# Performance work log

Measured on AMD Instinct MI355X. Metric: run time of the kernel, lower is better.

Reference implementation:

```python
import jax, jax.numpy as jnp
import numpy as np

H = 128
EPS = 1e-5

def _layernorm(x, g, b):
    mu = jnp.mean(x, axis=-1, keepdims=True)
    var = jnp.mean(jnp.square(x - mu), axis=-1, keepdims=True)
    return (x - mu) * jax.lax.rsqrt(var + EPS) * g + b

def _block(x, W, b, g, be):
    # Linear -> LayerNorm -> ReLU (dropout is identity at eval)
    return jax.nn.relu(_layernorm(x @ W + b, g, be))

def setup_inputs() -> dict:
    key = jax.random.key(0)
    ks = jax.random.split(key, 12)
    B, N, C = 32, 4096, 512
    s1 = 1.0 / np.sqrt(H)
    s2 = 1.0 / np.sqrt(2 * H)
    return {
        "fine_features": jax.random.normal(ks[0], (B, N, H), jnp.float32),
        "coarse_features": jax.random.normal(ks[1], (B, C, H), jnp.float32),
        "global_features": jax.random.normal(ks[2], (B, N, H), jnp.float32),
        "atom_to_coarse": jax.random.randint(ks[3], (B, N), 0, 600),  # some >= C (invalid)
        "W_pool": jax.random.uniform(ks[4], (H, H), jnp.float32, -s1, s1),
        "b_pool": jnp.zeros((H,), jnp.float32),
        "g_pool": jnp.ones((H,), jnp.float32),
        "be_pool": jnp.zeros((H,), jnp.float32),
        "W_unpool": jax.random.uniform(ks[5], (H, H), jnp.float32, -s1, s1),
        "b_unpool": jnp.zeros((H,), jnp.float32),
        "g_unpool": jnp.ones((H,), jnp.float32),
        "be_unpool": jnp.zeros((H,), jnp.float32),
        "W_gate": jax.random.uniform(ks[6], (2 * H, H), jnp.float32, -s2, s2),
        "b_gate": jnp.zeros((H,), jnp.float32),
        "W_glob": jax.random.uniform(ks[7], (2 * H, H), jnp.float32, -s2, s2),
        "b_glob": jnp.zeros((H,), jnp.float32),
        "g_glob": jnp.ones((H,), jnp.float32),
        "be_glob": jnp.zeros((H,), jnp.float32),
    }

def reference(fine_features, coarse_features, global_features, atom_to_coarse,
              W_pool, b_pool, g_pool, be_pool,
              W_unpool, b_unpool, g_unpool, be_unpool,
              W_gate, b_gate, W_glob, b_glob, g_glob, be_glob):
    B, N, Hd = fine_features.shape
    C = coarse_features.shape[1]
    idx = atom_to_coarse
    valid = (idx >= 0) & (idx < C)                      # [B,N]

    # ---- batched scatter-add pooling via flat segment_sum ----
    # invalid atoms routed to extra bucket C per batch element
    seg = jnp.where(valid, idx, C) + jnp.arange(B, dtype=idx.dtype)[:, None] * (C + 1)
    pooled = jax.ops.segment_sum(fine_features.reshape(B * N, Hd),
                                 seg.reshape(-1), num_segments=B * (C + 1))
    pooled = pooled.reshape(B, C + 1, Hd)[:, :C]        # [B,C,H]
    counts = jax.ops.segment_sum(valid.reshape(-1).astype(jnp.float32),
                                 seg.reshape(-1), num_segments=B * (C + 1))
    counts = counts.reshape(B, C + 1)[:, :C]
    coarse_from_fine = pooled / jnp.maximum(counts, 1.0)[..., None]
    coarse_from_fine = _block(coarse_from_fine, W_pool, b_pool, g_pool, be_pool)

    # ---- gather unpooling ----
    safe = jnp.where(valid, idx, 0)
    gathered = jnp.take_along_axis(coarse_features, safe[:, :, None], axis=1)  # [B,N,H]
    fine_from_coarse = jnp.where(valid[..., None], gathered, 0.0)
    fine_from_coarse = _block(fine_from_coarse, W_unpool, b_unpool, g_unpool, be_unpool)

    # ---- gated fusion ----
    fine_gate = jax.nn.sigmoid(jnp.concatenate([fine_features, fine_from_coarse], -1) @ W_gate + b_gate)
    fine_updated = fine_gate * fine_features + (1.0 - fine_gate) * fine_from_coarse
    coarse_gate = jax.nn.sigmoid(jnp.concatenate([coarse_features, coarse_from_fine], -1) @ W_gate + b_gate)
    coarse_updated = coarse_gate * coarse_features + (1.0 - coarse_gate) * coarse_from_fine

    # ---- global injection ----
    fine_wg = _block(jnp.concatenate([fine_updated, global_features], -1), W_glob, b_glob, g_glob, be_glob)
    fine_updated = fine_updated + 0.1 * fine_wg
    glob_c = jnp.broadcast_to(jnp.mean(global_features, axis=1, keepdims=True), (B, C, Hd))
    coarse_wg = _block(jnp.concatenate([coarse_updated, glob_c], -1), W_glob, b_glob, g_glob, be_glob)
    coarse_updated = coarse_updated + 0.1 * coarse_wg
    return (fine_updated, coarse_updated)
```

## Files before the change

kernel.cpp:

```cpp
#include <hip/hip_runtime.h>

typedef __bf16 bf16;
typedef bf16 bf16x8 __attribute__((ext_vector_type(8)));
typedef float f32x4 __attribute__((ext_vector_type(4)));

#define TPP 512
#define TPM 256
#define UPAD 136

#define NPOOL 1024
#define NGM   512
#define NPREP 64
#define NM1   256
#define NM0   2048

__device__ inline unsigned short f2bf(float f){
  union{ bf16 h; unsigned short u; } v; v.h = (bf16)f; return v.u;
}
__device__ inline float bf2f(unsigned short u){
  union{ unsigned short u; bf16 h; } v; v.u = u; return (float)v.h;
}
__device__ inline unsigned int pk2(float a, float b){
  return (unsigned int)f2bf(a) | ((unsigned int)f2bf(b) << 16);
}
union BF8 { bf16x8 v; unsigned int u[4]; };
__device__ inline bf16x8 pack8(float4 a, float4 b){
  BF8 r; r.u[0] = pk2(a.x, a.y); r.u[1] = pk2(a.z, a.w);
  r.u[2] = pk2(b.x, b.y); r.u[3] = pk2(b.z, b.w); return r.v;
}

__device__ inline void gll16(const unsigned short* g, unsigned short* l){
  __builtin_amdgcn_global_load_lds(
      (const __attribute__((address_space(1))) unsigned int*)g,
      (__attribute__((address_space(3))) unsigned int*)l, 16, 0, 0);
}
__device__ inline void stage_win(const unsigned short* __restrict__ src,
                                 unsigned short* half, int tid){
#pragma unroll
  for (int i = 0; i < 4; ++i){
    int p = (tid + i*TPM)*8;
    gll16(src + p, half + p);
  }
}

__device__ inline void gemm_win(const bf16x8 a[2], const unsigned short* half,
                                f32x4 acc[8], int lane){
#pragma unroll
  for (int kk = 0; kk < 2; ++kk){
    bf16x8 av = a[kk];
#pragma unroll
    for (int n = 0; n < 8; ++n){
      bf16x8 bv = *(const bf16x8*)(half + (size_t)((n*2 + kk)*512) + lane*8);
      acc[n] = __builtin_amdgcn_mfma_f32_16x16x32_bf16(av, bv, acc[n], 0, 0, 0);
    }
  }
}

__device__ inline void rowstats(const f32x4 acc[8], const float bia[8],
                                float mean[4], float rstd[4]){
#pragma unroll
  for (int ri = 0; ri < 4; ++ri){
    float s = 0.f, q = 0.f;
#pragma unroll
    for (int n = 0; n < 8; ++n){
      float z = acc[n][ri] + bia[n];
      s += z; q += z*z;
    }
#pragma unroll
    for (int m = 1; m < 16; m <<= 1){ s += __shfl_xor(s, m); q += __shfl_xor(q, m); }
    mean[ri] = s * (1.f/128.f);
    float var = q * (1.f/128.f) - mean[ri]*mean[ri];
    rstd[ri] = rsqrtf(var + 1e-5f);
  }
}

struct PoolSh {
  int sidx[4096];
  int rows[4096];
  int cnt[16], off[17], woff[16];
};
struct GmeanSh { float4 part4[16][32]; };
union PreSh { PoolSh p; GmeanSh g; };

__device__ void pool_body(PoolSh& sh, int pid,
                          const float* __restrict__ fine,
                          const int* __restrict__ idx,
                          unsigned short* __restrict__ pooled){
  int b = pid >> 5, g = pid & 31;
  int c0 = g * 16;
  int tid = threadIdx.x;
  const int* idx_b = idx + b*4096;
#pragma unroll
  for (int i = 0; i < 2; ++i)
    ((int4*)sh.sidx)[tid + i*TPP] = ((const int4*)idx_b)[tid + i*TPP];
  if (tid < 16) sh.cnt[tid] = 0;
  __syncthreads();
  for (int i = tid; i < 4096; i += TPP){
    unsigned d = (unsigned)(sh.sidx[i] - c0);
    if (d < 16u) atomicAdd(&sh.cnt[d], 1);
  }
  __syncthreads();
  if (tid == 0){
    int s = 0;
#pragma unroll
    for (int j = 0; j < 16; ++j){ sh.off[j] = s; s += sh.cnt[j]; }
    sh.off[16] = s;
  }
  __syncthreads();
  if (tid < 16) sh.woff[tid] = sh.off[tid];
  __syncthreads();
  for (int i = tid; i < 4096; i += TPP){
    unsigned d = (unsigned)(sh.sidx[i] - c0);
    if (d < 16u){ int p = atomicAdd(&sh.woff[d], 1); sh.rows[p] = i; }
  }
  __syncthreads();
  int hw = tid >> 5, l32 = tid & 31;
  const float* fb = fine + (size_t)b*4096*128;
  int o0 = sh.off[hw], o1 = sh.off[hw+1];
  float4 s = {0.f, 0.f, 0.f, 0.f};
  int m = o0;
  for (; m + 3 < o1; m += 4){
    float4 v0 = *((const float4*)(fb + (size_t)sh.rows[m+0]*128) + l32);
    float4 v1 = *((const float4*)(fb + (size_t)sh.rows[m+1]*128) + l32);
    float4 v2 = *((const float4*)(fb + (size_t)sh.rows[m+2]*128) + l32);
    float4 v3 = *((const float4*)(fb + (size_t)sh.rows[m+3]*128) + l32);
    s.x += (v0.x + v1.x) + (v2.x + v3.x);
    s.y += (v0.y + v1.y) + (v2.y + v3.y);
    s.z += (v0.z + v1.z) + (v2.z + v3.z);
    s.w += (v0.w + v1.w) + (v2.w + v3.w);
  }
  for (; m < o1; ++m){
    float4 v = *((const float4*)(fb + (size_t)sh.rows[m]*128) + l32);
    s.x += v.x; s.y += v.y; s.z += v.z; s.w += v.w;
  }
  float inv = 1.f / fmaxf((float)(o1 - o0), 1.f);
  unsigned short* po = pooled + ((size_t)(b*512 + c0 + hw))*128 + l32*4;
  uint2 w2; w2.x = pk2(s.x*inv, s.y*inv); w2.y = pk2(s.z*inv, s.w*inv);
  *(uint2*)po = w2;
}

__device__ void gmean_body(GmeanSh& sh, int gid,
                           const float* __restrict__ glob,
                           float* __restrict__ gmean){
  int b = gid >> 4, ch = gid & 15;
  int tid = threadIdx.x;
  int c4 = tid & 31, rg = tid >> 5;
  const float* gb = glob + ((size_t)b*4096 + ch*256)*128;
  float4 a = {0.f, 0.f, 0.f, 0.f};
#pragma unroll
  for (int i = 0; i < 16; ++i){
    int r = rg + i*16;
    float4 v = *(const float4*)(gb + (size_t)r*128 + c4*4);
    a.x += v.x; a.y += v.y; a.z += v.z; a.w += v.w;
  }
  sh.part4[rg][c4] = a;
  __syncthreads();
  if (tid < 32){
    float4 s = sh.part4[0][tid];
#pragma unroll
    for (int g = 1; g < 16; ++g){
      float4 v = sh.part4[g][tid];
      s.x += v.x; s.y += v.y; s.z += v.z; s.w += v.w;
    }
    float* gm = gmean + b*128 + tid*4;
    atomicAdd(&gm[0], s.x); atomicAdd(&gm[1], s.y);
    atomicAdd(&gm[2], s.z); atomicAdd(&gm[3], s.w);
  }
}

__device__ void prep_body(int e,
                          const float* __restrict__ Wp, const float* __restrict__ Wu,
                          const float* __restrict__ Wg, const float* __restrict__ Wgl,
                          unsigned short* __restrict__ WfP, unsigned short* __restrict__ WfU,
                          unsigned short* __restrict__ WfG, unsigned short* __restrict__ WfGl){
  int j = e & 7, lane = (e >> 3) & 63, frag = e >> 9;
  int kk = frag & 1, nblk = (frag >> 1) & 7, c = frag >> 4;
  int il = lane & 15, lg = lane >> 4;
  int col = nblk*16 + il;
  int k = c*64 + kk*32 + lg*8 + j;
  if (e < 16384){
    WfP[e] = f2bf(Wp[k*128 + col]);
    WfU[e] = f2bf(Wu[k*128 + col]);
  }
  WfG[e]  = f2bf(Wg[k*128 + col]);
  WfGl[e] = f2bf(Wgl[k*128 + col]);
}

__global__ __launch_bounds__(TPP) void k_pre(
    const float* __restrict__ fine, const int* __restrict__ idx,
    const float* __restrict__ glob,
    const float* __restrict__ Wp, const float* __restrict__ Wu,
    const float* __restrict__ Wg, const float* __restrict__ Wgl,
    unsigned short* __restrict__ pooled, float* __restrict__ gmean,
    unsigned short* __restrict__ WfP, unsigned short* __restrict__ WfU,
    unsigned short* __restrict__ WfG, unsigned short* __restrict__ WfGl){
  __shared__ __align__(16) PreSh sh;
  int bid = blockIdx.x;
  if (bid < NPOOL)             pool_body(sh.p, bid, fine, idx, pooled);
  else if (bid < NPOOL + NGM)  gmean_body(sh.g, bid - NPOOL, glob, gmean);
  else                         prep_body((bid - NPOOL - NGM)*TPP + threadIdx.x,
                                         Wp, Wu, Wg, Wgl, WfP, WfU, WfG, WfGl);
}

struct MegaSh {
  unsigned short wb[2][8192];
  unsigned short ubuf[4][16*UPAD];
};
template<int PATH>
__device__ void mega_body(MegaSh& sh, int bid,
    const float* __restrict__ a_src,
    const float* __restrict__ gath_src,
    const unsigned short* __restrict__ x1b,
    const int* __restrict__ idx,
    const float* __restrict__ gsrc,
    float gscale,
    const unsigned short* __restrict__ Wf1, const float* __restrict__ b1,
    const float* __restrict__ g1, const float* __restrict__ be1,
    const unsigned short* __restrict__ WfG, const float* __restrict__ bG,
    const unsigned short* __restrict__ WfGl, const float* __restrict__ bGl,
    const float* __restrict__ gGl, const float* __restrict__ beGl,
    float* __restrict__ out)
{
  int tid = threadIdx.x;
  int wave = tid >> 6, lane = tid & 63;
  int il = lane & 15, lg = lane >> 4;
  int row0 = bid * 64 + wave * 16;
  int b = (PATH == 0) ? (row0 >> 12) : (row0 >> 9);
  unsigned short* u = sh.ubuf[wave];

  stage_win(Wf1, sh.wb[0], tid);
  bf16x8 a1[4];
  if (PATH == 0){
    int n0 = row0 & 4095;
    int ci = idx[b*4096 + n0 + il];
    bool valid = (unsigned)ci < 512u;
    const float* cr = gath_src + ((size_t)b*512 + (valid ? ci : 0))*128;
#pragma unroll
    for (int c = 0; c < 2; ++c)
#pragma unroll
      for (int kk = 0; kk < 2; ++kk){
        float4 f0 = {0.f,0.f,0.f,0.f}, f1 = {0.f,0.f,0.f,0.f};
        if (valid){
          f0 = *(const float4*)(cr + c*64 + kk*32 + lg*8);
          f1 = *(const float4*)(cr + c*64 + kk*32 + lg*8 + 4);
        }
        a1[c*2 + kk] = pack8(f0, f1);
      }
  } else {
    const unsigned short* pr = x1b + (size_t)(row0 + il)*128;
#pragma unroll
    for (int c = 0; c < 2; ++c)
#pragma unroll
      for (int kk = 0; kk < 2; ++kk)
        a1[c*2 + kk] = *(const bf16x8*)(pr + c*64 + kk*32 + lg*8);
  }
  __syncthreads();

  f32x4 acc[8] = {};
  bf16x8 af[2];
  float4 raw[8];
  const float* ar = a_src + (size_t)(row0 + il)*128;

  stage_win(Wf1 + 8192, sh.wb[1], tid);
  af[0] = a1[0]; af[1] = a1[1];
  gemm_win(af, sh.wb[0], acc, lane);
  __syncthreads();

  stage_win(WfG, sh.wb[0], tid);
  af[0] = a1[2]; af[1] = a1[3];
  gemm_win(af, sh.wb[1], acc, lane);
#pragma unroll
  for (int c = 0; c < 2; ++c)
#pragma unroll
    for (int kk = 0; kk < 2; ++kk){
      raw[(c*2+kk)*2+0] = *(const float4*)(ar + c*64 + kk*32 + lg*8);
      raw[(c*2+kk)*2+1] = *(const float4*)(ar + c*64 + kk*32 + lg*8 + 4);
    }
  {
    float bia[8], gmv[8], btv[8];
#pragma unroll
    for (int n = 0; n < 8; ++n){
      int col = n*16 + il;
      bia[n] = b1[col]; gmv[n] = g1[col]; btv[n] = be1[col];
    }
    float mean[4], rstd[4];
    rowstats(acc, bia, mean, rstd);
#pragma unroll
    for (int ri = 0; ri < 4; ++ri)
#pragma unroll
      for (int n = 0; n < 8; ++n){
        float z = acc[n][ri] + bia[n];
        float y = fmaxf((z - mean[ri])*rstd[ri]*gmv[n] + btv[n], 0.f);
        u[(lg*4 + ri)*UPAD + n*16 + il] = f2bf(y);
      }
  }
  __syncthreads();

  stage_win(WfG + 8192, sh.wb[1], tid);
#pragma unroll
  for (int n = 0; n < 8; ++n) acc[n] = (f32x4){0.f,0.f,0.f,0.f};
  af[0] = pack8(raw[0], raw[1]); af[1] = pack8(raw[2], raw[3]);
  gemm_win(af, sh.wb[0], acc, lane);
  __syncthreads();

  stage_win(WfG + 16384, sh.wb[0], tid);
  af[0] = pack8(raw[4], raw[5]); af[1] = pack8(raw[6], raw[7]);
  gemm_win(af, sh.wb[1], acc, lane);
  __syncthreads();

  stage_win(WfG + 24576, sh.wb[1], tid);
  if (PATH == 0){
    const float* gr = gsrc + (size_t)(row0 + il)*128;
#pragma unroll
    for (int c = 0; c < 2; ++c)
#pragma unroll
      for (int kk = 0; kk < 2; ++kk){
        raw[(c*2+kk)*2+0] = *(const float4*)(gr + c*64 + kk*32 + lg*8);
        raw[(c*2+kk)*2+1] = *(const float4*)(gr + c*64 + kk*32 + lg*8 + 4);
      }
  } else {
    const float* gm = gsrc + b*128;
#pragma unroll
    for (int c = 0; c < 2; ++c)
#pragma unroll
      for (int kk = 0; kk < 2; ++kk){
        float4 f0 = *(const float4*)(gm + c*64 + kk*32 + lg*8);
        float4 f1 = *(const float4*)(gm + c*64 + kk*32 + lg*8 + 4);
        raw[(c*2+kk)*2+0] = (float4){f0.x*gscale, f0.y*gscale, f0.z*gscale, f0.w*gscale};
        raw[(c*2+kk)*2+1] = (float4){f1.x*gscale, f1.y*gscale, f1.z*gscale, f1.w*gscale};
      }
  }
  af[0] = *(const bf16x8*)(u + il*UPAD + 0*64 + 0*32 + lg*8);
  af[1] = *(const bf16x8*)(u + il*UPAD + 0*64 + 1*32 + lg*8);
  gemm_win(af, sh.wb[0], acc, lane);
  __syncthreads();

  stage_win(WfGl, sh.wb[0], tid);
  af[0] = *(const bf16x8*)(u + il*UPAD + 1*64 + 0*32 + lg*8);
  af[1] = *(const bf16x8*)(u + il*UPAD + 1*64 + 1*32 + lg*8);
  gemm_win(af, sh.wb[1], acc, lane);
#pragma unroll
  for (int ri = 0; ri < 4; ++ri){
    int grow = (row0 + lg*4 + ri)*128;
#pragma unroll
    for (int n = 0; n < 8; ++n){
      int col = n*16 + il;
      float z = acc[n][ri] + bG[col];
      float gt = 1.f / (1.f + __expf(-z));
      float f  = a_src[(size_t)grow + col];
      int ua = (lg*4 + ri)*UPAD + col;
      float u1 = bf2f(u[ua]);
      u[ua] = f2bf(gt*f + (1.f - gt)*u1);
    }
  }
  __syncthreads();

  stage_win(WfGl + 8192, sh.wb[1], tid);
#pragma unroll
  for (int n = 0; n < 8; ++n) acc[n] = (f32x4){0.f,0.f,0.f,0.f};
  af[0] = *(const bf16x8*)(u + il*UPAD + 0*64 + 0*32 + lg*8);
  af[1] = *(const bf16x8*)(u + il*UPAD + 0*64 + 1*32 + lg*8);
  gemm_win(af, sh.wb[0], acc, lane);
  __syncthreads();

  stage_win(WfGl + 16384, sh.wb[0], tid);
  af[0] = *(const bf16x8*)(u + il*UPAD + 1*64 + 0*32 + lg*8);
  af[1] = *(const bf16x8*)(u + il*UPAD + 1*64 + 1*32 + lg*8);
  gemm_win(af, sh.wb[1], acc, lane);
  __syncthreads();

  stage_win(WfGl + 24576, sh.wb[1], tid);
  af[0] = pack8(raw[0], raw[1]); af[1] = pack8(raw[2], raw[3]);
  gemm_win(af, sh.wb[0], acc, lane);
  __syncthreads();

  af[0] = pack8(raw[4], raw[5]); af[1] = pack8(raw[6], raw[7]);
  gemm_win(af, sh.wb[1], acc, lane);
  {
    float bia[8], gmv[8], btv[8];
#pragma unroll
    for (int n = 0; n < 8; ++n){
      int col = n*16 + il;
      bia[n] = bGl[col]; gmv[n] = gGl[col]; btv[n] = beGl[col];
    }
    float mean[4], rstd[4];
    rowstats(acc, bia, mean, rstd);
#pragma unroll
    for (int ri = 0; ri < 4; ++ri){
      int grow = (row0 + lg*4 + ri)*128;
#pragma unroll
      for (int n = 0; n < 8; ++n){
        int col = n*16 + il;
        float z = acc[n][ri] + bia[n];
        float y = fmaxf((z - mean[ri])*rstd[ri]*gmv[n] + btv[n], 0.f);
        float u2 = bf2f(u[(lg*4 + ri)*UPAD + col]);
        out[(size_t)grow + col] = u2 + 0.1f*y;
      }
    }
  }
}

__global__ __launch_bounds__(TPM, 3) void k_mega(
    const float* __restrict__ fine,
    const float* __restrict__ coarse,
    const int* __restrict__ idx,
    const float* __restrict__ glob,
    const unsigned short* __restrict__ pooled,
    const float* __restrict__ gmean,
    const unsigned short* __restrict__ WfP, const float* __restrict__ bP,
    const float* __restrict__ gP, const float* __restrict__ beP,
    const unsigned short* __restrict__ WfU, const float* __restrict__ bU,
    const float* __restrict__ gU, const float* __restrict__ beU,
    const unsigned short* __restrict__ WfG, const float* __restrict__ bG,
    const unsigned short* __restrict__ WfGl, const float* __restrict__ bGl,
    const float* __restrict__ gGl, const float* __restrict__ beGl,
    float* __restrict__ out_fine,
    float* __restrict__ out_coarse)
{
  __shared__ __align__(16) MegaSh sh;
  int bid = blockIdx.x;
  if (bid < NM1){
    mega_body<1>(sh, bid, coarse, nullptr, pooled, nullptr, gmean, 1.f/4096.f,
                 WfP, bP, gP, beP, WfG, bG, WfGl, bGl, gGl, beGl, out_coarse);
  } else {
    mega_body<0>(sh, bid - NM1, fine, coarse, nullptr, idx, glob, 1.0f,
                 WfU, bU, gU, beU, WfG, bG, WfGl, bGl, gGl, beGl, out_fine);
  }
}

extern "C" void kernel_launch(void* const* d_in, const int* in_sizes, int n_in,
                              void* d_out, int out_size, void* d_ws, size_t ws_size,
                              hipStream_t stream){
  const float* fine    = (const float*)d_in[0];
  const float* coarse  = (const float*)d_in[1];
  const float* glob    = (const float*)d_in[2];
  const int*   idx     = (const int*)  d_in[3];
  const float* W_pool  = (const float*)d_in[4];
  const float* b_pool  = (const float*)d_in[5];
  const float* g_pool  = (const float*)d_in[6];
  const float* be_pool = (const float*)d_in[7];
  const float* W_unpool  = (const float*)d_in[8];
  const float* b_unpool  = (const float*)d_in[9];
  const float* g_unpool  = (const float*)d_in[10];
  const float* be_unpool = (const float*)d_in[11];
  const float* W_gate = (const float*)d_in[12];
  const float* b_gate = (const float*)d_in[13];
  const float* W_glob = (const float*)d_in[14];
  const float* b_glob = (const float*)d_in[15];
  const float* g_glob = (const float*)d_in[16];
  const float* be_glob= (const float*)d_in[17];

  const int B = 32, N = 4096, C = 512;
  float* out_fine   = (float*)d_out;
  float* out_coarse = out_fine + (size_t)B*N*128;

  char* w = (char*)d_ws;
  unsigned short* WfP  = (unsigned short*)w; w += 16384*2;
  unsigned short* WfU  = (unsigned short*)w; w += 16384*2;
  unsigned short* WfG  = (unsigned short*)w; w += 32768*2;
  unsigned short* WfGl = (unsigned short*)w; w += 32768*2;
  float* gmean = (float*)w;                  w += B*128*4;
  unsigned short* pooled = (unsigned short*)w; w += (size_t)B*C*128*2;

  hipMemsetAsync(gmean, 0, B*128*4, stream);
  k_pre<<<NPOOL + NGM + NPREP, TPP, 0, stream>>>(
      fine, idx, glob, W_pool, W_unpool, W_gate, W_glob,
      pooled, gmean, WfP, WfU, WfG, WfGl);

  k_mega<<<NM1 + NM0, TPM, 0, stream>>>(
      fine, coarse, idx, glob, pooled, gmean,
      WfP, b_pool, g_pool, be_pool,
      WfU, b_unpool, g_unpool, be_unpool,
      WfG, b_gate, WfGl, b_glob, g_glob, be_glob,
      out_fine, out_coarse);
}
```

Before: 98.89 us.

## Overlap pooling and global mean with fine path; split coarse into trailing kernel

Weight prep moves into its own small kernel. The scatter pooling and global-mean reduction are folded into the main kernel as extra blocks scheduled after the fine-path blocks, so they share the GPU with the fine work instead of running as a separate dependent stage. The coarse path, which needs the pooled data and the global mean, moves to its own trailing kernel. Pool blocks now handle 64 clusters each with 256 threads, which cuts the redundant index scans. The cost is an extra launch and a longer serial loop per pool block.

```diff
diff --git a/kernel.cpp b/kernel.cpp
--- a/kernel.cpp
+++ b/kernel.cpp
@@ -4,15 +4,13 @@
 typedef bf16 bf16x8 __attribute__((ext_vector_type(8)));
 typedef float f32x4 __attribute__((ext_vector_type(4)));
 
-#define TPP 512
 #define TPM 256
 #define UPAD 136
 
-#define NPOOL 1024
-#define NGM   512
-#define NPREP 64
+#define NM0   2048
+#define NPB   256
+#define NGB   512
 #define NM1   256
-#define NM0   2048
 
 __device__ inline unsigned short f2bf(float f){
   union{ bf16 h; unsigned short u; } v; v.h = (bf16)f; return v.u;
@@ -77,66 +75,67 @@
 struct PoolSh {
   int sidx[4096];
   int rows[4096];
-  int cnt[16], off[17], woff[16];
+  int cnt[64], off[65], woff[64];
 };
-struct GmeanSh { float4 part4[16][32]; };
-union PreSh { PoolSh p; GmeanSh g; };
+struct GmeanSh { float4 part4[8][32]; };
 
 __device__ void pool_body(PoolSh& sh, int pid,
                           const float* __restrict__ fine,
                           const int* __restrict__ idx,
                           unsigned short* __restrict__ pooled){
-  int b = pid >> 5, g = pid & 31;
-  int c0 = g * 16;
+  int b = pid >> 3, g = pid & 7;
+  int c0 = g * 64;
   int tid = threadIdx.x;
   const int* idx_b = idx + b*4096;
 #pragma unroll
-  for (int i = 0; i < 2; ++i)
-    ((int4*)sh.sidx)[tid + i*TPP] = ((const int4*)idx_b)[tid + i*TPP];
-  if (tid < 16) sh.cnt[tid] = 0;
-  __syncthreads();
-  for (int i = tid; i < 4096; i += TPP){
+  for (int i = 0; i < 4; ++i)
+    ((int4*)sh.sidx)[tid + i*TPM] = ((const int4*)idx_b)[tid + i*TPM];
+  if (tid < 64) sh.cnt[tid] = 0;
+  __syncthreads();
+  for (int i = tid; i < 4096; i += TPM){
     unsigned d = (unsigned)(sh.sidx[i] - c0);
-    if (d < 16u) atomicAdd(&sh.cnt[d], 1);
+    if (d < 64u) atomicAdd(&sh.cnt[d], 1);
   }
   __syncthreads();
   if (tid == 0){
     int s = 0;
-#pragma unroll
-    for (int j = 0; j < 16; ++j){ sh.off[j] = s; s += sh.cnt[j]; }
-    sh.off[16] = s;
-  }
-  __syncthreads();
-  if (tid < 16) sh.woff[tid] = sh.off[tid];
-  __syncthreads();
-  for (int i = tid; i < 4096; i += TPP){
+    for (int j = 0; j < 64; ++j){ sh.off[j] = s; s += sh.cnt[j]; }
+    sh.off[64] = s;
+  }
+  __syncthreads();
+  if (tid < 64) sh.woff[tid] = sh.off[tid];
+  __syncthreads();
+  for (int i = tid; i < 4096; i += TPM){
     unsigned d = (unsigned)(sh.sidx[i] - c0);
-    if (d < 16u){ int p = atomicAdd(&sh.woff[d], 1); sh.rows[p] = i; }
+    if (d < 64u){ int p = atomicAdd(&sh.woff[d], 1); sh.rows[p] = i; }
   }
   __syncthreads();
   int hw = tid >> 5, l32 = tid & 31;
   const float* fb = fine + (size_t)b*4096*128;
-  int o0 = sh.off[hw], o1 = sh.off[hw+1];
-  float4 s = {0.f, 0.f, 0.f, 0.f};
-  int m = o0;
-  for (; m + 3 < o1; m += 4){
-    float4 v0 = *((const float4*)(fb + (size_t)sh.rows[m+0]*128) + l32);
-    float4 v1 = *((const float4*)(fb + (size_t)sh.rows[m+1]*128) + l32);
-    float4 v2 = *((const float4*)(fb + (size_t)sh.rows[m+2]*128) + l32);
-    float4 v3 = *((const float4*)(fb + (size_t)sh.rows[m+3]*128) + l32);
-    s.x += (v0.x + v1.x) + (v2.x + v3.x);
-    s.y += (v0.y + v1.y) + (v2.y + v3.y);
-    s.z += (v0.z + v1.z) + (v2.z + v3.z);
-    s.w += (v0.w + v1.w) + (v2.w + v3.w);
-  }
-  for (; m < o1; ++m){
-    float4 v = *((const float4*)(fb + (size_t)sh.rows[m]*128) + l32);
-    s.x += v.x; s.y += v.y; s.z += v.z; s.w += v.w;
-  }
-  float inv = 1.f / fmaxf((float)(o1 - o0), 1.f);
-  unsigned short* po = pooled + ((size_t)(b*512 + c0 + hw))*128 + l32*4;
-  uint2 w2; w2.x = pk2(s.x*inv, s.y*inv); w2.y = pk2(s.z*inv, s.w*inv);
-  *(uint2*)po = w2;
+  for (int s8 = 0; s8 < 8; ++s8){
+    int cl = hw + s8*8;
+    int o0 = sh.off[cl], o1 = sh.off[cl+1];
+    float4 s = {0.f, 0.f, 0.f, 0.f};
+    int m = o0;
+    for (; m + 3 < o1; m += 4){
+      float4 v0 = *((const float4*)(fb + (size_t)sh.rows[m+0]*128) + l32);
+      float4 v1 = *((const float4*)(fb + (size_t)sh.rows[m+1]*128) + l32);
+      float4 v2 = *((const float4*)(fb + (size_t)sh.rows[m+2]*128) + l32);
+      float4 v3 = *((const float4*)(fb + (size_t)sh.rows[m+3]*128) + l32);
+      s.x += (v0.x + v1.x) + (v2.x + v3.x);
+      s.y += (v0.y + v1.y) + (v2.y + v3.y);
+      s.z += (v0.z + v1.z) + (v2.z + v3.z);
+      s.w += (v0.w + v1.w) + (v2.w + v3.w);
+    }
+    for (; m < o1; ++m){
+      float4 v = *((const float4*)(fb + (size_t)sh.rows[m]*128) + l32);
+      s.x += v.x; s.y += v.y; s.z += v.z; s.w += v.w;
+    }
+    float inv = 1.f / fmaxf((float)(o1 - o0), 1.f);
+    unsigned short* po = pooled + ((size_t)(b*512 + c0 + cl))*128 + l32*4;
+    uint2 w2; w2.x = pk2(s.x*inv, s.y*inv); w2.y = pk2(s.z*inv, s.w*inv);
+    *(uint2*)po = w2;
+  }
 }
 
 __device__ void gmean_body(GmeanSh& sh, int gid,
@@ -148,8 +147,8 @@
   const float* gb = glob + ((size_t)b*4096 + ch*256)*128;
   float4 a = {0.f, 0.f, 0.f, 0.f};
 #pragma unroll
-  for (int i = 0; i < 16; ++i){
-    int r = rg + i*16;
+  for (int i = 0; i < 32; ++i){
+    int r = rg + i*8;
     float4 v = *(const float4*)(gb + (size_t)r*128 + c4*4);
     a.x += v.x; a.y += v.y; a.z += v.z; a.w += v.w;
   }
@@ -158,7 +157,7 @@
   if (tid < 32){
     float4 s = sh.part4[0][tid];
 #pragma unroll
-    for (int g = 1; g < 16; ++g){
+    for (int g = 1; g < 8; ++g){
       float4 v = sh.part4[g][tid];
       s.x += v.x; s.y += v.y; s.z += v.z; s.w += v.w;
     }
@@ -168,11 +167,12 @@
   }
 }
 
-__device__ void prep_body(int e,
-                          const float* __restrict__ Wp, const float* __restrict__ Wu,
-                          const float* __restrict__ Wg, const float* __restrict__ Wgl,
-                          unsigned short* __restrict__ WfP, unsigned short* __restrict__ WfU,
-                          unsigned short* __restrict__ WfG, unsigned short* __restrict__ WfGl){
+__global__ __launch_bounds__(TPM) void k_prep(
+    const float* __restrict__ Wp, const float* __restrict__ Wu,
+    const float* __restrict__ Wg, const float* __restrict__ Wgl,
+    unsigned short* __restrict__ WfP, unsigned short* __restrict__ WfU,
+    unsigned short* __restrict__ WfG, unsigned short* __restrict__ WfGl){
+  int e = blockIdx.x * TPM + threadIdx.x;
   int j = e & 7, lane = (e >> 3) & 63, frag = e >> 9;
   int kk = frag & 1, nblk = (frag >> 1) & 7, c = frag >> 4;
   int il = lane & 15, lg = lane >> 4;
@@ -184,22 +184,6 @@
   }
   WfG[e]  = f2bf(Wg[k*128 + col]);
   WfGl[e] = f2bf(Wgl[k*128 + col]);
-}
-
-__global__ __launch_bounds__(TPP) void k_pre(
-    const float* __restrict__ fine, const int* __restrict__ idx,
-    const float* __restrict__ glob,
-    const float* __restrict__ Wp, const float* __restrict__ Wu,
-    const float* __restrict__ Wg, const float* __restrict__ Wgl,
-    unsigned short* __restrict__ pooled, float* __restrict__ gmean,
-    unsigned short* __restrict__ WfP, unsigned short* __restrict__ WfU,
-    unsigned short* __restrict__ WfG, unsigned short* __restrict__ WfGl){
-  __shared__ __align__(16) PreSh sh;
-  int bid = blockIdx.x;
-  if (bid < NPOOL)             pool_body(sh.p, bid, fine, idx, pooled);
-  else if (bid < NPOOL + NGM)  gmean_body(sh.g, bid - NPOOL, glob, gmean);
-  else                         prep_body((bid - NPOOL - NGM)*TPP + threadIdx.x,
-                                         Wp, Wu, Wg, Wgl, WfP, WfU, WfG, WfGl);
 }
 
 struct MegaSh {
@@ -400,32 +384,48 @@
   }
 }
 
-__global__ __launch_bounds__(TPM, 3) void k_mega(
+union MainSh { MegaSh m; PoolSh p; GmeanSh g; };
+
+__global__ __launch_bounds__(TPM, 3) void k_main(
     const float* __restrict__ fine,
     const float* __restrict__ coarse,
     const int* __restrict__ idx,
     const float* __restrict__ glob,
-    const unsigned short* __restrict__ pooled,
-    const float* __restrict__ gmean,
-    const unsigned short* __restrict__ WfP, const float* __restrict__ bP,
-    const float* __restrict__ gP, const float* __restrict__ beP,
     const unsigned short* __restrict__ WfU, const float* __restrict__ bU,
     const float* __restrict__ gU, const float* __restrict__ beU,
     const unsigned short* __restrict__ WfG, const float* __restrict__ bG,
     const unsigned short* __restrict__ WfGl, const float* __restrict__ bGl,
     const float* __restrict__ gGl, const float* __restrict__ beGl,
-    float* __restrict__ out_fine,
+    unsigned short* __restrict__ pooled,
+    float* __restrict__ gmean,
+    float* __restrict__ out_fine)
+{
+  __shared__ __align__(16) MainSh sh;
+  int bid = blockIdx.x;
+  if (bid < NM0){
+    mega_body<0>(sh.m, bid, fine, coarse, nullptr, idx, glob, 1.0f,
+                 WfU, bU, gU, beU, WfG, bG, WfGl, bGl, gGl, beGl, out_fine);
+  } else if (bid < NM0 + NPB){
+    pool_body(sh.p, bid - NM0, fine, idx, pooled);
+  } else {
+    gmean_body(sh.g, bid - NM0 - NPB, glob, gmean);
+  }
+}
+
+__global__ __launch_bounds__(TPM, 3) void k_coarse(
+    const float* __restrict__ coarse,
+    const unsigned short* __restrict__ pooled,
+    const float* __restrict__ gmean,
+    const unsigned short* __restrict__ WfP, const float* __restrict__ bP,
+    const float* __restrict__ gP, const float* __restrict__ beP,
+    const unsigned short* __restrict__ WfG, const float* __restrict__ bG,
+    const unsigned short* __restrict__ WfGl, const float* __restrict__ bGl,
+    const float* __restrict__ gGl, const float* __restrict__ beGl,
     float* __restrict__ out_coarse)
 {
   __shared__ __align__(16) MegaSh sh;
-  int bid = blockIdx.x;
-  if (bid < NM1){
-    mega_body<1>(sh, bid, coarse, nullptr, pooled, nullptr, gmean, 1.f/4096.f,
-                 WfP, bP, gP, beP, WfG, bG, WfGl, bGl, gGl, beGl, out_coarse);
-  } else {
-    mega_body<0>(sh, bid - NM1, fine, coarse, nullptr, idx, glob, 1.0f,
-                 WfU, bU, gU, beU, WfG, bG, WfGl, bGl, gGl, beGl, out_fine);
-  }
+  mega_body<1>(sh, blockIdx.x, coarse, nullptr, pooled, nullptr, gmean, 1.f/4096.f,
+               WfP, bP, gP, beP, WfG, bG, WfGl, bGl, gGl, beGl, out_coarse);
 }
 
 extern "C" void kernel_launch(void* const* d_in, const int* in_sizes, int n_in,
@@ -463,14 +463,17 @@
   unsigned short* pooled = (unsigned short*)w; w += (size_t)B*C*128*2;
 
   hipMemsetAsync(gmean, 0, B*128*4, stream);
-  k_pre<<<NPOOL + NGM + NPREP, TPP, 0, stream>>>(
-      fine, idx, glob, W_pool, W_unpool, W_gate, W_glob,
-      pooled, gmean, WfP, WfU, WfG, WfGl);
-
-  k_mega<<<NM1 + NM0, TPM, 0, stream>>>(
-      fine, coarse, idx, glob, pooled, gmean,
-      WfP, b_pool, g_pool, be_pool,
+  k_prep<<<128, TPM, 0, stream>>>(W_pool, W_unpool, W_gate, W_glob, WfP, WfU, WfG, WfGl);
+
+  k_main<<<NM0 + NPB + NGB, TPM, 0, stream>>>(
+      fine, coarse, idx, glob,
       WfU, b_unpool, g_unpool, be_unpool,
       WfG, b_gate, WfGl, b_glob, g_glob, be_glob,
-      out_fine, out_coarse);
-}
+      pooled, gmean, out_fine);
+
+  k_coarse<<<NM1, TPM, 0, stream>>>(
+      coarse, pooled, gmean,
+      WfP, b_pool, g_pool, be_pool,
+      WfG, b_gate, WfGl, b_glob, g_glob, be_glob,
+      out_coarse);
+}
```

New measurement: 106.5 us. 7.7% more time.
